# Kernel optimization log

Hardware: AMD Instinct MI355X
Metric: run time of the kernel (lower is better)

The kernel has to match this reference:

```python
import jax, jax.numpy as jnp
import numpy as np

B, T = 4, 15
NY = NX = 256
RES = 0.05
LAT0 = 32.0
G = 9.81
F0 = 1e-4
C0 = 2.7
DT = 21600.0
TINT = 86400.0
NSTEP = int(TINT // DT)  # 4 Euler sub-steps

# --- grid spacing: mean of dx, dy as in lonlat2dxdy (uniform lon/lat grid) ---
_lat = LAT0 + RES * np.arange(NX, dtype=np.float64)  # lat varies along axis 1
_dx_mean = RES * 111000.0
_dy_mean = RES * 111000.0 * np.mean(np.cos(np.deg2rad(_lat)))
DX = np.float32(0.5 * (_dx_mean + _dy_mean))

# --- Helmholtz operator in DST-I space, shape (NY-2, NX-2) (square grid) ---
_i = np.arange(1, NX - 1, dtype=np.float64)
_j = np.arange(1, NY - 1, dtype=np.float64)
_X, _Y = np.meshgrid(_i, _j, indexing='ij')
_lap = (2 * (np.cos(np.pi / (NX - 1) * _X) - 1) / DX**2
        + 2 * (np.cos(np.pi / (NY - 1) * _Y) - 1) / DX**2)
HELM = jnp.asarray((G / F0) * _lap - G * F0 / C0**2, dtype=jnp.float32)

# --- boundary masks (SSH=None -> no NaN land mask; ind0 is empty) ---
_m = np.full((NY, NX), 3, dtype=np.int32)
_m[0, :] = _m[:, 0] = _m[-1, :] = _m[:, -1] = 1
_m[1, 1:-1] = 2; _m[1:-1, 1] = 2
_m[-2, 1:-1] = 2; _m[-3, 1:-1] = 2
_m[1:-1, -2] = 2; _m[1:-1, -3] = 2
IND12 = jnp.asarray((_m == 1) | (_m == 2))


def dstI1D(x):
    """1D type-I discrete sine transform along last axis."""
    n = x.shape[-1]
    xp = jnp.pad(x, [(0, 0)] * (x.ndim - 1) + [(1, 1)])
    return jnp.fft.irfft(-1j * xp, norm='ortho')[..., 1:n + 1]


def dstI2D(x):
    return jnp.swapaxes(dstI1D(jnp.swapaxes(dstI1D(x), -1, -2)), -1, -2)


def h2uv(h):
    """SSH -> geostrophic (u, v). f is the constant F0."""
    u = jnp.zeros_like(h).at[..., 1:-1, 1:].set(
        -G / F0 * (h[..., 2:, :-1] + h[..., 2:, 1:] - h[..., :-2, 1:] - h[..., :-2, :-1]) / (4 * DX))
    v = jnp.zeros_like(h).at[..., 1:, 1:-1].set(
        G / F0 * (h[..., 1:, 2:] + h[..., :-1, 2:] - h[..., :-1, :-2] - h[..., 1:, :-2]) / (4 * DX))
    return u, v


def h2pv(h, hbc):
    """SSH -> potential vorticity with boundary values from hbc on ind1|ind2."""
    interior = (G / F0 * ((h[..., 2:, 1:-1] + h[..., :-2, 1:-1] - 2 * h[..., 1:-1, 1:-1]) / DX**2
                          + (h[..., 1:-1, 2:] + h[..., 1:-1, :-2] - 2 * h[..., 1:-1, 1:-1]) / DX**2)
                - G * F0 / C0**2 * h[..., 1:-1, 1:-1])
    q = jnp.zeros_like(h).at[..., 1:-1, 1:-1].set(interior)
    return jnp.where(IND12, -G * F0 / C0**2 * hbc, q)


def _adv(up, vp, um, vm, v0):
    """3rd-order upwind advection."""
    c = 1.0 / (6 * DX)
    inner = (
        -up[..., 1:-1, 1:-1] * c * (2 * v0[..., 2:-2, 3:-1] + 3 * v0[..., 2:-2, 2:-2] - 6 * v0[..., 2:-2, 1:-3] + v0[..., 2:-2, :-4])
        + um[..., 1:-1, 1:-1] * c * (v0[..., 2:-2, 4:] - 6 * v0[..., 2:-2, 3:-1] + 3 * v0[..., 2:-2, 2:-2] + 2 * v0[..., 2:-2, 1:-3])
        - vp[..., 1:-1, 1:-1] * c * (2 * v0[..., 3:-1, 2:-2] + 3 * v0[..., 2:-2, 2:-2] - 6 * v0[..., 1:-3, 2:-2] + v0[..., :-4, 2:-2])
        + vm[..., 1:-1, 1:-1] * c * (v0[..., 4:, 2:-2] - 6 * v0[..., 3:-1, 2:-2] + 3 * v0[..., 2:-2, 2:-2] + 2 * v0[..., 1:-3, 2:-2]))
    return jnp.zeros_like(v0).at[..., 2:-2, 2:-2].set(inner)


def rhs(u, v, q0, way=1.0):
    uT = way * 0.5 * (u[..., 1:-1, 1:-1] + u[..., 1:-1, 2:])
    vT = way * 0.5 * (v[..., 1:-1, 1:-1] + v[..., 2:, 1:-1])
    up = jnp.maximum(uT, 0.0); um = jnp.minimum(uT, 0.0)
    vp = jnp.maximum(vT, 0.0); vm = jnp.minimum(vT, 0.0)
    r = _adv(up, vp, um, vm, q0)
    # beta term is identically zero: f = F0 is spatially constant. Kdiffus=None.
    return jnp.where(IND12, 0.0, r)


def pv2h(q, hb, qb):
    """PV -> SSH via DST-based inverse Helmholtz solve."""
    qin = q[..., 1:-1, 1:-1] - qb[..., 1:-1, 1:-1]
    inv = dstI2D(dstI2D(qin) / HELM)
    return jnp.zeros_like(q).at[..., 1:-1, 1:-1].set(inv) + hb


def conv2d(x, w, b):
    y = jax.lax.conv_general_dilated(x, w, (1, 1), 'SAME',
                                     dimension_numbers=('NCHW', 'OIHW', 'NCHW'))
    return y + b[None, :, None, None]


def qg_forecast(x):
    """One-day QG forecast of each frame from the previous one (NSTEP Euler sub-steps)."""
    h0 = x[:, :-1]            # [B, T-1, NY, NX]
    hb = h0                    # background / boundary SSH
    qb = h2pv(hb, hb)

    def body(carry, _):
        h, q = carry
        u, v = h2uv(h)
        q1 = q + DT * rhs(u, v, q)
        h1 = pv2h(q1, hb, qb)
        return (h1, q1), None

    (hf, _), _ = jax.lax.scan(body, (h0, qb), None, length=NSTEP)
    return hf


def setup_inputs() -> dict:
    key = jax.random.key(0)
    ks = jax.random.split(key, 8)
    s = 0.05
    return {
        'x': jax.random.normal(ks[0], (B, T, NY, NX), jnp.float32),
        'w_in': s * jax.random.normal(ks[1], (64, T, 3, 3), jnp.float32),
        'b_in': jnp.zeros((64,), jnp.float32),
        'w_hid': s * jax.random.normal(ks[2], (64, 64, 3, 3), jnp.float32),
        'b_hid': jnp.zeros((64,), jnp.float32),
        'w_b1': s * jax.random.normal(ks[3], (64, 64, 3, 3), jnp.float32),
        'b_b1': jnp.zeros((64,), jnp.float32),
        'w_b21': s * jax.random.normal(ks[4], (64, 64, 3, 3), jnp.float32),
        'b_b21': jnp.zeros((64,), jnp.float32),
        'w_b22': s * jax.random.normal(ks[5], (64, 64, 3, 3), jnp.float32),
        'b_b22': jnp.zeros((64,), jnp.float32),
        'w_out': s * jax.random.normal(ks[6], (T, 128, 3, 3), jnp.float32),
        'b_out': jnp.zeros((T,), jnp.float32),
    }


def reference(x, w_in, b_in, w_hid, b_hid, w_b1, b_b1, w_b21, b_b21,
              w_b22, b_b22, w_out, b_out):
    # QG dynamical prior cost
    hf = qg_forecast(x)
    dyn_cost = jnp.mean((x[:, 1:] - hf) ** 2)
    # bilinear AE prior cost (bilin_quad=False -> product of two branches)
    z = conv2d(x, w_in, b_in)
    z = conv2d(jax.nn.relu(z), w_hid, b_hid)
    nonlin = conv2d(z, w_b21, b_b21) * conv2d(z, w_b22, b_b22)
    xa = conv2d(jnp.concatenate([conv2d(z, w_b1, b_b1), nonlin], axis=1), w_out, b_out)
    ae_cost = jnp.mean((x - xa) ** 2)
    return dyn_cost + ae_cost
```

## Files before the change

kernel.cpp:

```cpp
#include <hip/hip_runtime.h>
#include <math.h>

#define NS 56
#define NPIX 65536
#define NB_RED 1024

static constexpr double D_PI = 3.14159265358979323846;

typedef __attribute__((ext_vector_type(8))) short short8;
typedef __attribute__((ext_vector_type(4))) float f32x4;
typedef __attribute__((ext_vector_type(16))) float f32x16;

__device__ inline unsigned short f2bf(float f) {
  union { float f; unsigned int u; } v; v.f = f;
  unsigned int r = v.u + 0x7FFFu + ((v.u >> 16) & 1u);
  return (unsigned short)(r >> 16);
}
__device__ inline float bf2f(unsigned short b) {
  union { float f; unsigned int u; } v; v.u = ((unsigned int)b) << 16;
  return v.f;
}

#define OFF_PART 0
#define OFF_S    4096
#define OFF_HM   (OFF_S + 32768)
#define OFF_H    (OFF_HM + 65536)
#define SLC      (NS * NPIX)
#define OFF_Q0   (OFF_H + SLC)
#define OFF_Q1   (OFF_Q0 + SLC)
#define OFF_QB   (OFF_Q1 + SLC)
#define OFF_TA   (OFF_QB + SLC)
#define OFF_U    (OFF_TA + SLC / 2)
#define OFF_V    (OFF_U + SLC / 2)
#define OFF_XP   OFF_H
#define OFF_Z1   (OFF_XP + 2097152)
#define OFF_Z2   (OFF_Z1 + 8388608)
#define OFF_BC   (OFF_Z2 + 8388608)
#define OFF_XA   (OFF_BC + 8388608)
#define OFF_WT   (OFF_XA + 2097152)
#define W_IN    0
#define W_HID   10240
#define W_B1    47104
#define W_B21   83968
#define W_B22   120832
#define W_O1    157696
#define W_O2    166912

#define QCLAMP 1.0e12f
#define HCLAMP 1.0e15f

__global__ __launch_bounds__(256) void k_dst_init(unsigned short* __restrict__ S,
                                                  float* __restrict__ HM, float dx2f) {
  int idx = blockIdx.x * 256 + threadIdx.x;
  int i = idx >> 8, j = idx & 255;
  float sv = 0.f, hv = 1.f;
  if (i < 254 && j < 254) {
    double arg = D_PI * (double)((i + 1) * (j + 1)) / 255.0;
    sv = (float)((2.0 / sqrt(510.0)) * sin(arg));
    double la = 2.0 * (cos(D_PI * (double)(i + 1) / 255.0) - 1.0) / (double)dx2f
              + 2.0 * (cos(D_PI * (double)(j + 1) / 255.0) - 1.0) / (double)dx2f;
    hv = (float)((9.81 / 1e-4) * la - 9.81 * 1e-4 / (2.7 * 2.7));
  }
  S[idx] = f2bf(sv);
  HM[idx] = hv;
}

__global__ __launch_bounds__(256) void k_qg_init(const float* __restrict__ x,
                                                 float* __restrict__ h,
                                                 float* __restrict__ q,
                                                 float* __restrict__ qb,
                                                 float dx2, float gf, float gfc) {
  int idx = blockIdx.x * 256 + threadIdx.x;
  int s = idx >> 16, p = idx & 65535;
  int y = p >> 8, xx = p & 255;
  int b = s / 14, t = s - b * 14;
  const float* hb = x + (size_t)(b * 15 + t) * NPIX;
  float hc = hb[p];
  float qv;
  if (y >= 2 && y <= 252 && xx >= 2 && xx <= 252) {
    qv = gf * ((hb[p + 256] + hb[p - 256] - 2.f * hc) / dx2
             + (hb[p + 1] + hb[p - 1] - 2.f * hc) / dx2) - gfc * hc;
  } else {
    qv = -gfc * hc;
  }
  h[idx] = hc;
  q[idx] = qv;
  qb[idx] = qv;
}

__global__ __launch_bounds__(256) void k_qrhs(const float* __restrict__ h,
                                              const float* __restrict__ qc,
                                              const float* __restrict__ qb,
                                              float* __restrict__ qn,
                                              unsigned short* __restrict__ tA,
                                              float ngf, float pgf, float fdx,
                                              float cc, float dtf) {
  int idx = blockIdx.x * 256 + threadIdx.x;
  int s = idx >> 16, p = idx & 65535;
  int y = p >> 8, xx = p & 255;
  const float* H = h + (size_t)s * NPIX;
  const float* Q = qc + (size_t)s * NPIX;
  float qv = Q[p];
  float q1 = qv;
  if (y >= 2 && y <= 252 && xx >= 2 && xx <= 252) {
    float hSW = H[p + 255], hS = H[p + 256], hSE = H[p + 257];
    float hNW = H[p - 257], hN = H[p - 256], hNE = H[p - 255];
    float hW = H[p - 1], hE = H[p + 1];
    float uA = ngf * (hSW + hS - hN - hNW) / fdx;
    float uB = ngf * (hS + hSE - hNE - hN) / fdx;
    float vA = pgf * (hE + hNE - hNW - hW) / fdx;
    float vB = pgf * (hSE + hE - hW - hSW) / fdx;
    float uT = 0.5f * (uA + uB);
    float vT = 0.5f * (vA + vB);
    float up = fmaxf(uT, 0.f), um = fminf(uT, 0.f);
    float vp = fmaxf(vT, 0.f), vm = fminf(vT, 0.f);
    float Q0 = qv;
    float QE = Q[p + 1], QW = Q[p - 1], QEE = Q[p + 2], QWW = Q[p - 2];
    float QS = Q[p + 256], QN = Q[p - 256], QSS = Q[p + 512], QNN = Q[p - 512];
    float r = -up * cc * (2.f * QE + 3.f * Q0 - 6.f * QW + QWW)
            + um * cc * (QEE - 6.f * QE + 3.f * Q0 + 2.f * QW)
            - vp * cc * (2.f * QS + 3.f * Q0 - 6.f * QN + QNN)
            + vm * cc * (QSS - 6.f * QS + 3.f * Q0 + 2.f * QN);
    q1 = qv + dtf * r;
    q1 = fminf(fmaxf(q1, -QCLAMP), QCLAMP);
  }
  qn[idx] = q1;
  int wy = (y == 0) ? 254 : ((y == 255) ? 255 : y - 1);
  int wx = (xx == 0) ? 254 : ((xx == 255) ? 255 : xx - 1);
  float val = 0.f;
  if (y >= 1 && y <= 254 && xx >= 1 && xx <= 254) val = q1 - qb[idx];
  tA[(size_t)s * NPIX + wy * 256 + wx] = f2bf(val);
}

template <int EPI>
__global__ __launch_bounds__(512) void k_solve(const unsigned short* __restrict__ Sm,
                                               const unsigned short* __restrict__ Xb,
                                               unsigned short* __restrict__ Ob,
                                               const float* __restrict__ HM,
                                               const float* __restrict__ xin,
                                               float* __restrict__ hout) {
  __shared__ unsigned short Ul[32 * 256];
  const int s = blockIdx.x, q = blockIdx.y;
  const unsigned short* X = Xb + (size_t)s * NPIX;
  const int lane = threadIdx.x & 63, w = threadIdx.x >> 6;
  const int r31 = lane & 31, kh = lane >> 5;

  f32x16 acc;
#pragma unroll
  for (int i = 0; i < 16; ++i) acc[i] = 0.f;
  {
    const int ar = (32 * q + r31) * 256;
    const int br = (32 * w + r31) * 256;
#pragma unroll 4
    for (int kc = 0; kc < 256; kc += 16) {
      short8 a = *(const short8*)&Sm[ar + kc + kh * 8];
      short8 b = *(const short8*)&X[br + kc + kh * 8];
      acc = __builtin_amdgcn_mfma_f32_32x32x16_bf16(a, b, acc, 0, 0, 0);
    }
  }
  {
    const int col = 32 * w + r31;
    const int g = col >> 3, c7 = col & 7;
#pragma unroll
    for (int reg = 0; reg < 16; ++reg) {
      int i = (reg & 3) + 8 * (reg >> 2) + 4 * kh;
      Ul[i * 256 + (((g ^ (i & 7)) << 3) | c7)] = f2bf(acc[reg]);
    }
  }
  __syncthreads();

  f32x16 acc2;
#pragma unroll
  for (int i = 0; i < 16; ++i) acc2[i] = 0.f;
  {
    const int ar = (32 * w + r31) * 256;
    const int urow = r31 * 256;
    const int x7 = (r31 & 7);
#pragma unroll 4
    for (int kc = 0; kc < 256; kc += 16) {
      int g0 = (kc >> 3) + kh;
      short8 a = *(const short8*)&Sm[ar + kc + kh * 8];
      short8 b = *(const short8*)&Ul[urow + ((g0 ^ x7) << 3)];
      acc2 = __builtin_amdgcn_mfma_f32_32x32x16_bf16(a, b, acc2, 0, 0, 0);
    }
  }
  const int gn = 32 * q + r31;
  if (EPI == 0) {
    unsigned short* O = Ob + (size_t)s * NPIX;
#pragma unroll
    for (int reg = 0; reg < 16; ++reg) {
      int gm = 32 * w + (reg & 3) + 8 * (reg >> 2) + 4 * kh;
      O[(size_t)gm * 256 + gn] = f2bf(acc2[reg] / HM[(size_t)gm * 256 + gn]);
    }
  } else {
    int b = s / 14, t = s - b * 14;
    const float* hb = xin + (size_t)(b * 15 + t) * NPIX;
    float* H = hout + (size_t)s * NPIX;
    if (gn < 254) {
#pragma unroll
      for (int reg = 0; reg < 16; ++reg) {
        int gm = 32 * w + (reg & 3) + 8 * (reg >> 2) + 4 * kh;
        if (gm < 254) {
          size_t o = (size_t)(gm + 1) * 256 + (gn + 1);
          float hv = acc2[reg] + hb[o];
          H[o] = fminf(fmaxf(hv, -HCLAMP), HCLAMP);
        }
      }
    }
  }
}

__global__ __launch_bounds__(256) void k_pack_x(const float* __restrict__ x,
                                                unsigned short* __restrict__ xp) {
  int e = blockIdx.x * 256 + threadIdx.x;
  int b = e >> 16, p = e & 65535;
  const float* xb = x + (size_t)b * 15 * NPIX + p;
  union { unsigned short u16[16]; uint4 u4[2]; } vv;
#pragma unroll
  for (int c = 0; c < 15; ++c) vv.u16[c] = f2bf(xb[(size_t)c * NPIX]);
  vv.u16[15] = 0;
  uint4* dst = (uint4*)&xp[(size_t)e * 16];
  dst[0] = vv.u4[0];
  dst[1] = vv.u4[1];
}

__global__ __launch_bounds__(256) void k_wprep_all(const float* __restrict__ w_in,
                                                   const float* __restrict__ w_hid,
                                                   const float* __restrict__ w_b1,
                                                   const float* __restrict__ w_b21,
                                                   const float* __restrict__ w_b22,
                                                   const float* __restrict__ w_out,
                                                   unsigned short* __restrict__ wtb) {
  const int job = blockIdx.y;
  const float* src;
  int dstOff, chunks, icpShift, icw, ic0, icReal, ocw, ocReal;
  switch (job) {
    case 0: src = w_in;  dstOff = W_IN;  chunks = 5;  icpShift = 4; icw = 15;  ic0 = 0;  icReal = 15; ocw = 64; ocReal = 64; break;
    case 1: src = w_hid; dstOff = W_HID; chunks = 18; icpShift = 6; icw = 64;  ic0 = 0;  icReal = 64; ocw = 64; ocReal = 64; break;
    case 2: src = w_b1;  dstOff = W_B1;  chunks = 18; icpShift = 6; icw = 64;  ic0 = 0;  icReal = 64; ocw = 64; ocReal = 64; break;
    case 3: src = w_b21; dstOff = W_B21; chunks = 18; icpShift = 6; icw = 64;  ic0 = 0;  icReal = 64; ocw = 64; ocReal = 64; break;
    case 4: src = w_b22; dstOff = W_B22; chunks = 18; icpShift = 6; icw = 64;  ic0 = 0;  icReal = 64; ocw = 64; ocReal = 64; break;
    case 5: src = w_out; dstOff = W_O1;  chunks = 18; icpShift = 6; icw = 128; ic0 = 0;  icReal = 64; ocw = 16; ocReal = 15; break;
    default: src = w_out; dstOff = W_O2; chunks = 18; icpShift = 6; icw = 128; ic0 = 64; icReal = 64; ocw = 16; ocReal = 15; break;
  }
  int e = blockIdx.x * 256 + threadIdx.x;
  int total = chunks * 4 * ocw * 8;
  if (e >= total) return;
  int j = e & 7;
  int oc = (e >> 3) % ocw;
  int ckg = e / (8 * ocw);
  int kg = ckg & 3, c = ckg >> 2;
  int Kidx = c * 32 + kg * 8 + j;
  int tap = Kidx >> icpShift;
  int ic = Kidx & ((1 << icpShift) - 1);
  float v = 0.f;
  if (tap < 9 && ic < icReal && oc < ocReal)
    v = src[((size_t)oc * icw + ic0 + ic) * 9 + tap];
  wtb[dstOff + e] = f2bf(v);
}

template <int NSRC, int NOC, int OCF, bool RELU, int EMODE>
__global__ __launch_bounds__(256) void k_conv64(const unsigned short* __restrict__ in0,
                                                const unsigned short* __restrict__ in1,
                                                const unsigned short* __restrict__ wt,
                                                const float* __restrict__ bias, int ocReal,
                                                const unsigned short* __restrict__ other,
                                                unsigned short* __restrict__ out) {
  constexpr int OCW = NOC * 16;
  __shared__ unsigned short tile[324 * 64];

  const int tid = threadIdx.x;
  const int lane = tid & 63, wave = tid >> 6;
  const int cl = lane & 15, kg = lane >> 4;
  const int b = blockIdx.z;
  const int gx0 = blockIdx.x * 16, gy0 = blockIdx.y * 16;

  f32x4 acc[4][NOC];
#pragma unroll
  for (int j = 0; j < NOC; ++j) {
    int oc = j * 16 + cl;
    float bv = (bias != nullptr && oc < ocReal) ? bias[oc] : 0.f;
#pragma unroll
    for (int i = 0; i < 4; ++i) acc[i][j] = (f32x4){bv, bv, bv, bv};
  }

  for (int src = 0; src < NSRC; ++src) {
    const unsigned short* inb = (src ? in1 : in0) + (size_t)b * NPIX * 64;
    const unsigned short* wtp = wt + src * 36864;
    if (src) __syncthreads();
    for (int c = tid; c < 2592; c += 256) {
      int pp = c >> 3, g = c & 7;
      int ly = pp / 18, lx = pp - ly * 18;
      int iy = gy0 + ly - 1, ix = gx0 + lx - 1;
      uint4 v = make_uint4(0u, 0u, 0u, 0u);
      if (iy >= 0 && iy < 256 && ix >= 0 && ix < 256)
        v = *(const uint4*)&inb[((size_t)iy * 256 + ix) * 64 + g * 8];
      int sw = g ^ (pp & 7);
      *(uint4*)&tile[pp * 64 + sw * 8] = v;
    }
    __syncthreads();
#pragma unroll 3
    for (int cm = 0; cm < 18; ++cm) {
      const int tap = cm >> 1;
      const int g = (cm & 1) * 4 + kg;
      const int dy = tap / 3, dxx = tap - dy * 3;
      short8 bfr[NOC];
#pragma unroll
      for (int j = 0; j < NOC; ++j)
        bfr[j] = *(const short8*)&wtp[(((size_t)cm * 4 + kg) * OCW + j * 16 + cl) * 8];
      const int tc = cl + dxx;
#pragma unroll
      for (int i = 0; i < 4; ++i) {
        int pp = (wave * 4 + i + dy) * 18 + tc;
        int g2 = g ^ (pp & 7);
        short8 av = *(const short8*)&tile[pp * 64 + g2 * 8];
#pragma unroll
        for (int j = 0; j < NOC; ++j)
          acc[i][j] = __builtin_amdgcn_mfma_f32_16x16x32_bf16(av, bfr[j], acc[i][j], 0, 0, 0);
      }
    }
  }

  const size_t outBase = (size_t)b * NPIX * OCF;
#pragma unroll
  for (int i = 0; i < 4; ++i) {
    int y = gy0 + wave * 4 + i;
#pragma unroll
    for (int j = 0; j < NOC; ++j) {
      int oc = j * 16 + cl;
#pragma unroll
      for (int r = 0; r < 4; ++r) {
        int px = gx0 + kg * 4 + r;
        size_t oi = outBase + ((size_t)y * 256 + px) * OCF + oc;
        float v = acc[i][j][r];
        if (EMODE == 1) v *= bf2f(other[oi]);
        if (RELU) v = fmaxf(v, 0.f);
        out[oi] = f2bf(v);
      }
    }
  }
}

__global__ __launch_bounds__(256) void k_conv16(const unsigned short* __restrict__ in,
                                                const unsigned short* __restrict__ wt,
                                                const float* __restrict__ bias,
                                                unsigned short* __restrict__ out) {
  __shared__ unsigned short wlds[10240];
  __shared__ unsigned short tile[324 * 16];

  const int tid = threadIdx.x;
  const int lane = tid & 63, wave = tid >> 6;
  const int cl = lane & 15, kg = lane >> 4;
  const int b = blockIdx.z;
  const int gx0 = blockIdx.x * 16, gy0 = blockIdx.y * 16;

  {
    uint4* wl = (uint4*)wlds;
    const uint4* wg = (const uint4*)wt;
    for (int i = tid; i < 1280; i += 256) wl[i] = wg[i];
  }
  const unsigned short* inb = in + (size_t)b * NPIX * 16;
  for (int c = tid; c < 648; c += 256) {
    int pp = c >> 1, g = c & 1;
    int ly = pp / 18, lx = pp - ly * 18;
    int iy = gy0 + ly - 1, ix = gx0 + lx - 1;
    uint4 v = make_uint4(0u, 0u, 0u, 0u);
    if (iy >= 0 && iy < 256 && ix >= 0 && ix < 256)
      v = *(const uint4*)&inb[((size_t)iy * 256 + ix) * 16 + g * 8];
    int sw = g ^ (pp & 1);
    *(uint4*)&tile[pp * 16 + sw * 8] = v;
  }
  __syncthreads();

  f32x4 acc[4][4];
#pragma unroll
  for (int j = 0; j < 4; ++j) {
    float bv = bias[j * 16 + cl];
#pragma unroll
    for (int i = 0; i < 4; ++i) acc[i][j] = (f32x4){bv, bv, bv, bv};
  }

#pragma unroll
  for (int c = 0; c < 5; ++c) {
    int tap = 2 * c + (kg >> 1);
    int dy = tap / 3, dxx = tap - dy * 3;
    int gidx = kg & 1;
    short8 bfr[4];
#pragma unroll
    for (int j = 0; j < 4; ++j)
      bfr[j] = *(const short8*)&wlds[((c * 4 + kg) * 64 + j * 16 + cl) * 8];
    int tc = cl + dxx;
#pragma unroll
    for (int i = 0; i < 4; ++i) {
      int tr = wave * 4 + i + dy;
      if (tr > 17) tr = 17;
      int pp = tr * 18 + tc;
      int g2 = gidx ^ (pp & 1);
      short8 av = *(const short8*)&tile[pp * 16 + g2 * 8];
#pragma unroll
      for (int j = 0; j < 4; ++j)
        acc[i][j] = __builtin_amdgcn_mfma_f32_16x16x32_bf16(av, bfr[j], acc[i][j], 0, 0, 0);
    }
  }

  const size_t outBase = (size_t)b * NPIX * 64;
#pragma unroll
  for (int i = 0; i < 4; ++i) {
    int y = gy0 + wave * 4 + i;
#pragma unroll
    for (int j = 0; j < 4; ++j) {
      int oc = j * 16 + cl;
#pragma unroll
      for (int r = 0; r < 4; ++r) {
        int px = gx0 + kg * 4 + r;
        size_t oi = outBase + ((size_t)y * 256 + px) * 64 + oc;
        out[oi] = f2bf(fmaxf(acc[i][j][r], 0.f));
      }
    }
  }
}

__global__ __launch_bounds__(256) void k_red_dyn(const float* __restrict__ x,
                                                 const float* __restrict__ h,
                                                 double* __restrict__ part) {
  double sum = 0.0;
  for (int e = blockIdx.x * 256 + threadIdx.x; e < NS * NPIX; e += NB_RED * 256) {
    int s = e >> 16, p = e & 65535;
    int b = s / 14, t = s - b * 14;
    float d = x[(size_t)(b * 15 + t + 1) * NPIX + p] - h[e];
    sum += (double)d * (double)d;
  }
  for (int o = 32; o > 0; o >>= 1) sum += __shfl_down(sum, o);
  __shared__ double sw[4];
  int lane = threadIdx.x & 63, wid = threadIdx.x >> 6;
  if (lane == 0) sw[wid] = sum;
  __syncthreads();
  if (threadIdx.x == 0) part[blockIdx.x] = sw[0] + sw[1] + sw[2] + sw[3];
}

__global__ __launch_bounds__(256) void k_red_ae(const float* __restrict__ x,
                                                const unsigned short* __restrict__ xa,
                                                double* __restrict__ part) {
  double sum = 0.0;
  for (int e = blockIdx.x * 256 + threadIdx.x; e < 60 * NPIX; e += NB_RED * 256) {
    int b = e / (15 * NPIX);
    int r2 = e - b * 15 * NPIX;
    int c = r2 >> 16, p = r2 & 65535;
    float xav = bf2f(xa[((size_t)b * NPIX + p) * 16 + c]);
    float d = x[e] - xav;
    sum += (double)d * (double)d;
  }
  for (int o = 32; o > 0; o >>= 1) sum += __shfl_down(sum, o);
  __shared__ double sw[4];
  int lane = threadIdx.x & 63, wid = threadIdx.x >> 6;
  if (lane == 0) sw[wid] = sum;
  __syncthreads();
  if (threadIdx.x == 0) part[NB_RED + blockIdx.x] = sw[0] + sw[1] + sw[2] + sw[3];
}

__global__ __launch_bounds__(256) void k_final(const double* __restrict__ part,
                                               float* __restrict__ out) {
  double s1 = 0.0, s2 = 0.0;
  for (int i = threadIdx.x; i < NB_RED; i += 256) {
    s1 += part[i];
    s2 += part[NB_RED + i];
  }
  for (int o = 32; o > 0; o >>= 1) {
    s1 += __shfl_down(s1, o);
    s2 += __shfl_down(s2, o);
  }
  __shared__ double a1[4], a2[4];
  int lane = threadIdx.x & 63, wid = threadIdx.x >> 6;
  if (lane == 0) { a1[wid] = s1; a2[wid] = s2; }
  __syncthreads();
  if (threadIdx.x == 0) {
    double v = (a1[0] + a1[1] + a1[2] + a1[3]) / (double)(NS * NPIX)
             + (a2[0] + a2[1] + a2[2] + a2[3]) / (double)(60 * NPIX);
    if (!(v == v)) v = 0.0;
    if (v > 1.0e30) v = 1.0e30;
    if (v < -1.0e30) v = -1.0e30;
    out[0] = (float)v;
  }
}

extern "C" void kernel_launch(void* const* d_in, const int* in_sizes, int n_in,
                              void* d_out, int out_size, void* d_ws, size_t ws_size,
                              hipStream_t stream) {
  (void)in_sizes; (void)n_in; (void)out_size; (void)ws_size;
  const float* x     = (const float*)d_in[0];
  const float* w_in  = (const float*)d_in[1];
  const float* b_in  = (const float*)d_in[2];
  const float* w_hid = (const float*)d_in[3];
  const float* b_hid = (const float*)d_in[4];
  const float* w_b1  = (const float*)d_in[5];
  const float* b_b1  = (const float*)d_in[6];
  const float* w_b21 = (const float*)d_in[7];
  const float* b_b21 = (const float*)d_in[8];
  const float* w_b22 = (const float*)d_in[9];
  const float* b_b22 = (const float*)d_in[10];
  const float* w_out = (const float*)d_in[11];
  const float* b_out = (const float*)d_in[12];
  float* ws = (float*)d_ws;
  float* out = (float*)d_out;

  double mc = 0.0;
  for (int k = 0; k < 256; ++k) mc += cos((32.0 + 0.05 * k) * D_PI / 180.0);
  mc /= 256.0;
  float DXf = (float)(0.5 * (5550.0 + 5550.0 * mc));
  float dx2 = DXf * DXf;
  float gf  = (float)(9.81 / 1e-4);
  float ngf = (float)(-9.81 / 1e-4);
  float gfc = (float)(9.81 * 1e-4 / (2.7 * 2.7));
  float fdx = 4.0f * DXf;
  float cc  = 1.0f / (6.0f * DXf);
  float dtf = 21600.0f;

  double* part = (double*)d_ws;
  unsigned short* S  = (unsigned short*)(ws + OFF_S);
  float* HM = ws + OFF_HM;
  float* h  = ws + OFF_H;
  float* q0 = ws + OFF_Q0;
  float* q1 = ws + OFF_Q1;
  float* qb = ws + OFF_QB;
  unsigned short* tA = (unsigned short*)(ws + OFF_TA);
  unsigned short* A1 = (unsigned short*)(ws + OFF_U);
  unsigned short* wtb = (unsigned short*)(ws + OFF_WT);

  k_dst_init<<<dim3(256), dim3(256), 0, stream>>>(S, HM, dx2);
  k_wprep_all<<<dim3(144, 7), dim3(256), 0, stream>>>(w_in, w_hid, w_b1, w_b21, w_b22, w_out, wtb);
  k_qg_init<<<dim3(NS * NPIX / 256), dim3(256), 0, stream>>>(x, h, q0, qb, dx2, gf, gfc);

  float* qc = q0;
  float* qn = q1;
  dim3 sg(56, 8);
  for (int step = 0; step < 4; ++step) {
    k_qrhs<<<dim3(NS * NPIX / 256), dim3(256), 0, stream>>>(h, qc, qb, qn, tA,
                                                            ngf, gf, fdx, cc, dtf);
    k_solve<0><<<sg, dim3(512), 0, stream>>>(S, tA, A1, HM, nullptr, nullptr);
    k_solve<1><<<sg, dim3(512), 0, stream>>>(S, A1, nullptr, nullptr, x, h);
    float* tmp = qc; qc = qn; qn = tmp;
  }
  k_red_dyn<<<dim3(NB_RED), dim3(256), 0, stream>>>(x, h, part);

  unsigned short* xp = (unsigned short*)(ws + OFF_XP);
  unsigned short* z1 = (unsigned short*)(ws + OFF_Z1);
  unsigned short* z2 = (unsigned short*)(ws + OFF_Z2);
  unsigned short* bc = (unsigned short*)(ws + OFF_BC);
  unsigned short* xa = (unsigned short*)(ws + OFF_XA);

  k_pack_x<<<dim3(4 * NPIX / 256), dim3(256), 0, stream>>>(x, xp);

  dim3 cg4(16, 16, 4);
  k_conv16<<<cg4, dim3(256), 0, stream>>>(xp, wtb + W_IN, b_in, z1);
  k_conv64<1, 4, 64, false, 0><<<cg4, dim3(256), 0, stream>>>(
      z1, z1, wtb + W_HID, b_hid, 64, nullptr, z2);
  k_conv64<1, 4, 64, false, 0><<<cg4, dim3(256), 0, stream>>>(
      z2, z2, wtb + W_B1, b_b1, 64, nullptr, z1);
  k_conv64<1, 4, 64, false, 0><<<cg4, dim3(256), 0, stream>>>(
      z2, z2, wtb + W_B21, b_b21, 64, nullptr, bc);
  k_conv64<1, 4, 64, false, 1><<<cg4, dim3(256), 0, stream>>>(
      z2, z2, wtb + W_B22, b_b22, 64, bc, bc);
  k_conv64<2, 1, 16, false, 0><<<cg4, dim3(256), 0, stream>>>(
      z1, bc, wtb + W_O1, b_out, 15, nullptr, xa);

  k_red_ae<<<dim3(NB_RED), dim3(256), 0, stream>>>(x, xa, part);
  k_final<<<dim3(1), dim3(256), 0, stream>>>(part, out);
}
```

Baseline: 525.8 us.

## Fuse setup kernels, carry bf16 q-deltas, fuse bilinear convs and reductions

Merges the DST table init, weight prep, QG init and input packing into one preamble launch. The Euler loop no longer keeps full fp32 q arrays: it reconstructs q from the base PV plus the bf16 delta that the solve already consumes, which cuts memory traffic but stores the evolving q state at bf16 precision. The two bilinear-branch convolutions are fused into one kernel that shares the input tile and multiplies the results in registers, and the final reductions become a single kernel that finishes with a last-block atomic counter. The second-source weight stride of the output conv is also corrected from 36864 to 9216.

```diff
diff --git a/kernel.cpp b/kernel.cpp
--- a/kernel.cpp
+++ b/kernel.cpp
@@ -3,7 +3,6 @@
 
 #define NS 56
 #define NPIX 65536
-#define NB_RED 1024
 
 static constexpr double D_PI = 3.14159265358979323846;
 
@@ -21,18 +20,17 @@
   return v.f;
 }
 
+#define SLC      (NS * NPIX)
 #define OFF_PART 0
+#define OFF_CNT  3584
 #define OFF_S    4096
-#define OFF_HM   (OFF_S + 32768)
-#define OFF_H    (OFF_HM + 65536)
-#define SLC      (NS * NPIX)
-#define OFF_Q0   (OFF_H + SLC)
-#define OFF_Q1   (OFF_Q0 + SLC)
-#define OFF_QB   (OFF_Q1 + SLC)
-#define OFF_TA   (OFF_QB + SLC)
-#define OFF_U    (OFF_TA + SLC / 2)
-#define OFF_V    (OFF_U + SLC / 2)
-#define OFF_XP   OFF_H
+#define OFF_HM   36864
+#define OFF_H    102400
+#define OFF_QB   (OFF_H + SLC)
+#define OFF_DQ0  (OFF_QB + SLC)
+#define OFF_DQ1  (OFF_DQ0 + SLC / 2)
+#define OFF_A1   (OFF_DQ1 + SLC / 2)
+#define OFF_XP   (OFF_A1 + SLC / 2)
 #define OFF_Z1   (OFF_XP + 2097152)
 #define OFF_Z2   (OFF_Z1 + 8388608)
 #define OFF_BC   (OFF_Z2 + 8388608)
@@ -49,59 +47,115 @@
 #define QCLAMP 1.0e12f
 #define HCLAMP 1.0e15f
 
-__global__ __launch_bounds__(256) void k_dst_init(unsigned short* __restrict__ S,
-                                                  float* __restrict__ HM, float dx2f) {
-  int idx = blockIdx.x * 256 + threadIdx.x;
-  int i = idx >> 8, j = idx & 255;
-  float sv = 0.f, hv = 1.f;
-  if (i < 254 && j < 254) {
-    double arg = D_PI * (double)((i + 1) * (j + 1)) / 255.0;
-    sv = (float)((2.0 / sqrt(510.0)) * sin(arg));
-    double la = 2.0 * (cos(D_PI * (double)(i + 1) / 255.0) - 1.0) / (double)dx2f
-              + 2.0 * (cos(D_PI * (double)(j + 1) / 255.0) - 1.0) / (double)dx2f;
-    hv = (float)((9.81 / 1e-4) * la - 9.81 * 1e-4 / (2.7 * 2.7));
-  }
-  S[idx] = f2bf(sv);
-  HM[idx] = hv;
-}
-
-__global__ __launch_bounds__(256) void k_qg_init(const float* __restrict__ x,
-                                                 float* __restrict__ h,
-                                                 float* __restrict__ q,
-                                                 float* __restrict__ qb,
-                                                 float dx2, float gf, float gfc) {
-  int idx = blockIdx.x * 256 + threadIdx.x;
-  int s = idx >> 16, p = idx & 65535;
-  int y = p >> 8, xx = p & 255;
-  int b = s / 14, t = s - b * 14;
-  const float* hb = x + (size_t)(b * 15 + t) * NPIX;
-  float hc = hb[p];
-  float qv;
-  if (y >= 2 && y <= 252 && xx >= 2 && xx <= 252) {
-    qv = gf * ((hb[p + 256] + hb[p - 256] - 2.f * hc) / dx2
-             + (hb[p + 1] + hb[p - 1] - 2.f * hc) / dx2) - gfc * hc;
+__global__ __launch_bounds__(256) void k_preamble(const float* __restrict__ x,
+                                                  const float* __restrict__ w_in,
+                                                  const float* __restrict__ w_hid,
+                                                  const float* __restrict__ w_b1,
+                                                  const float* __restrict__ w_b21,
+                                                  const float* __restrict__ w_b22,
+                                                  const float* __restrict__ w_out,
+                                                  unsigned short* __restrict__ S,
+                                                  float* __restrict__ HM,
+                                                  unsigned short* __restrict__ wtb,
+                                                  float* __restrict__ h,
+                                                  float* __restrict__ qb,
+                                                  unsigned short* __restrict__ xp,
+                                                  unsigned int* __restrict__ cnt,
+                                                  float dx2, float gf, float gfc) {
+  const int blk = blockIdx.x;
+  const int tid = threadIdx.x;
+  if (blk < 256) {
+    int idx = blk * 256 + tid;
+    if (idx == 0) *cnt = 0u;
+    int i = idx >> 8, j = idx & 255;
+    float sv = 0.f, hv = 1.f;
+    if (i < 254 && j < 254) {
+      double arg = D_PI * (double)((i + 1) * (j + 1)) / 255.0;
+      sv = (float)((2.0 / sqrt(510.0)) * sin(arg));
+      double la = 2.0 * (cos(D_PI * (double)(i + 1) / 255.0) - 1.0) / (double)dx2
+                + 2.0 * (cos(D_PI * (double)(j + 1) / 255.0) - 1.0) / (double)dx2;
+      hv = (float)((9.81 / 1e-4) * la - 9.81 * 1e-4 / (2.7 * 2.7));
+    }
+    S[idx] = f2bf(sv);
+    HM[idx] = hv;
+  } else if (blk < 256 + 1008) {
+    int jb = blk - 256;
+    int job = jb / 144;
+    int e = (jb - job * 144) * 256 + tid;
+    const float* src;
+    int dstOff, chunks, icpShift, icw, ic0, icReal, ocw, ocReal;
+    switch (job) {
+      case 0: src = w_in;  dstOff = W_IN;  chunks = 5;  icpShift = 4; icw = 15;  ic0 = 0;  icReal = 15; ocw = 64; ocReal = 64; break;
+      case 1: src = w_hid; dstOff = W_HID; chunks = 18; icpShift = 6; icw = 64;  ic0 = 0;  icReal = 64; ocw = 64; ocReal = 64; break;
+      case 2: src = w_b1;  dstOff = W_B1;  chunks = 18; icpShift = 6; icw = 64;  ic0 = 0;  icReal = 64; ocw = 64; ocReal = 64; break;
+      case 3: src = w_b21; dstOff = W_B21; chunks = 18; icpShift = 6; icw = 64;  ic0 = 0;  icReal = 64; ocw = 64; ocReal = 64; break;
+      case 4: src = w_b22; dstOff = W_B22; chunks = 18; icpShift = 6; icw = 64;  ic0 = 0;  icReal = 64; ocw = 64; ocReal = 64; break;
+      case 5: src = w_out; dstOff = W_O1;  chunks = 18; icpShift = 6; icw = 128; ic0 = 0;  icReal = 64; ocw = 16; ocReal = 15; break;
+      default: src = w_out; dstOff = W_O2; chunks = 18; icpShift = 6; icw = 128; ic0 = 64; icReal = 64; ocw = 16; ocReal = 15; break;
+    }
+    int total = chunks * 4 * ocw * 8;
+    if (e < total) {
+      int j = e & 7;
+      int oc = (e >> 3) % ocw;
+      int ckg = e / (8 * ocw);
+      int kg = ckg & 3, c = ckg >> 2;
+      int Kidx = c * 32 + kg * 8 + j;
+      int tap = Kidx >> icpShift;
+      int ic = Kidx & ((1 << icpShift) - 1);
+      float v = 0.f;
+      if (tap < 9 && ic < icReal && oc < ocReal)
+        v = src[((size_t)oc * icw + ic0 + ic) * 9 + tap];
+      wtb[dstOff + e] = f2bf(v);
+    }
+  } else if (blk < 256 + 1008 + 14336) {
+    int idx = (blk - 1264) * 256 + tid;
+    int s = idx >> 16, p = idx & 65535;
+    int y = p >> 8, xx = p & 255;
+    int b = s / 14, t = s - b * 14;
+    const float* hb = x + (size_t)(b * 15 + t) * NPIX;
+    float hc = hb[p];
+    float qv;
+    if (y >= 2 && y <= 252 && xx >= 2 && xx <= 252) {
+      qv = gf * ((hb[p + 256] + hb[p - 256] - 2.f * hc) / dx2
+               + (hb[p + 1] + hb[p - 1] - 2.f * hc) / dx2) - gfc * hc;
+    } else {
+      qv = -gfc * hc;
+    }
+    h[idx] = hc;
+    qb[idx] = qv;
   } else {
-    qv = -gfc * hc;
-  }
-  h[idx] = hc;
-  q[idx] = qv;
-  qb[idx] = qv;
-}
-
-__global__ __launch_bounds__(256) void k_qrhs(const float* __restrict__ h,
-                                              const float* __restrict__ qc,
-                                              const float* __restrict__ qb,
-                                              float* __restrict__ qn,
-                                              unsigned short* __restrict__ tA,
-                                              float ngf, float pgf, float fdx,
-                                              float cc, float dtf) {
+    int e = (blk - 15600) * 256 + tid;
+    int b = e >> 16, p = e & 65535;
+    const float* xb = x + (size_t)b * 15 * NPIX + p;
+    union { unsigned short u16[16]; uint4 u4[2]; } vv;
+#pragma unroll
+    for (int c = 0; c < 15; ++c) vv.u16[c] = f2bf(xb[(size_t)c * NPIX]);
+    vv.u16[15] = 0;
+    uint4* dst = (uint4*)&xp[(size_t)e * 16];
+    dst[0] = vv.u4[0];
+    dst[1] = vv.u4[1];
+  }
+}
+
+template <bool FIRST>
+__global__ __launch_bounds__(256) void k_qrhs_dq(const float* __restrict__ h,
+                                                 const float* __restrict__ qbb,
+                                                 const unsigned short* __restrict__ dqin,
+                                                 unsigned short* __restrict__ dqout,
+                                                 float ngf, float pgf, float fdx,
+                                                 float cc, float dtf) {
   int idx = blockIdx.x * 256 + threadIdx.x;
   int s = idx >> 16, p = idx & 65535;
   int y = p >> 8, xx = p & 255;
   const float* H = h + (size_t)s * NPIX;
-  const float* Q = qc + (size_t)s * NPIX;
-  float qv = Q[p];
-  float q1 = qv;
+  const float* QB = qbb + (size_t)s * NPIX;
+  const unsigned short* DQ = FIRST ? nullptr : dqin + (size_t)s * NPIX;
+  auto dq = [&](int yy, int xc) -> float {
+    if (FIRST) return 0.f;
+    if (yy < 1 || yy > 254 || xc < 1 || xc > 254) return 0.f;
+    return bf2f(DQ[(yy - 1) * 256 + (xc - 1)]);
+  };
+  float q1mqb = 0.f;
   if (y >= 2 && y <= 252 && xx >= 2 && xx <= 252) {
     float hSW = H[p + 255], hS = H[p + 256], hSE = H[p + 257];
     float hNW = H[p - 257], hN = H[p - 256], hNE = H[p - 255];
@@ -114,22 +168,23 @@
     float vT = 0.5f * (vA + vB);
     float up = fmaxf(uT, 0.f), um = fminf(uT, 0.f);
     float vp = fmaxf(vT, 0.f), vm = fminf(vT, 0.f);
-    float Q0 = qv;
-    float QE = Q[p + 1], QW = Q[p - 1], QEE = Q[p + 2], QWW = Q[p - 2];
-    float QS = Q[p + 256], QN = Q[p - 256], QSS = Q[p + 512], QNN = Q[p - 512];
+    float qbc = QB[p];
+    float Q0 = qbc + dq(y, xx);
+    float QE = QB[p + 1] + dq(y, xx + 1), QW = QB[p - 1] + dq(y, xx - 1);
+    float QEE = QB[p + 2] + dq(y, xx + 2), QWW = QB[p - 2] + dq(y, xx - 2);
+    float QS = QB[p + 256] + dq(y + 1, xx), QN = QB[p - 256] + dq(y - 1, xx);
+    float QSS = QB[p + 512] + dq(y + 2, xx), QNN = QB[p - 512] + dq(y - 2, xx);
     float r = -up * cc * (2.f * QE + 3.f * Q0 - 6.f * QW + QWW)
             + um * cc * (QEE - 6.f * QE + 3.f * Q0 + 2.f * QW)
             - vp * cc * (2.f * QS + 3.f * Q0 - 6.f * QN + QNN)
             + vm * cc * (QSS - 6.f * QS + 3.f * Q0 + 2.f * QN);
-    q1 = qv + dtf * r;
+    float q1 = Q0 + dtf * r;
     q1 = fminf(fmaxf(q1, -QCLAMP), QCLAMP);
-  }
-  qn[idx] = q1;
+    q1mqb = q1 - qbc;
+  }
   int wy = (y == 0) ? 254 : ((y == 255) ? 255 : y - 1);
   int wx = (xx == 0) ? 254 : ((xx == 255) ? 255 : xx - 1);
-  float val = 0.f;
-  if (y >= 1 && y <= 254 && xx >= 1 && xx <= 254) val = q1 - qb[idx];
-  tA[(size_t)s * NPIX + wy * 256 + wx] = f2bf(val);
+  dqout[(size_t)s * NPIX + wy * 256 + wx] = f2bf(q1mqb);
 }
 
 template <int EPI>
@@ -210,56 +265,7 @@
   }
 }
 
-__global__ __launch_bounds__(256) void k_pack_x(const float* __restrict__ x,
-                                                unsigned short* __restrict__ xp) {
-  int e = blockIdx.x * 256 + threadIdx.x;
-  int b = e >> 16, p = e & 65535;
-  const float* xb = x + (size_t)b * 15 * NPIX + p;
-  union { unsigned short u16[16]; uint4 u4[2]; } vv;
-#pragma unroll
-  for (int c = 0; c < 15; ++c) vv.u16[c] = f2bf(xb[(size_t)c * NPIX]);
-  vv.u16[15] = 0;
-  uint4* dst = (uint4*)&xp[(size_t)e * 16];
-  dst[0] = vv.u4[0];
-  dst[1] = vv.u4[1];
-}
-
-__global__ __launch_bounds__(256) void k_wprep_all(const float* __restrict__ w_in,
-                                                   const float* __restrict__ w_hid,
-                                                   const float* __restrict__ w_b1,
-                                                   const float* __restrict__ w_b21,
-                                                   const float* __restrict__ w_b22,
-                                                   const float* __restrict__ w_out,
-                                                   unsigned short* __restrict__ wtb) {
-  const int job = blockIdx.y;
-  const float* src;
-  int dstOff, chunks, icpShift, icw, ic0, icReal, ocw, ocReal;
-  switch (job) {
-    case 0: src = w_in;  dstOff = W_IN;  chunks = 5;  icpShift = 4; icw = 15;  ic0 = 0;  icReal = 15; ocw = 64; ocReal = 64; break;
-    case 1: src = w_hid; dstOff = W_HID; chunks = 18; icpShift = 6; icw = 64;  ic0 = 0;  icReal = 64; ocw = 64; ocReal = 64; break;
-    case 2: src = w_b1;  dstOff = W_B1;  chunks = 18; icpShift = 6; icw = 64;  ic0 = 0;  icReal = 64; ocw = 64; ocReal = 64; break;
-    case 3: src = w_b21; dstOff = W_B21; chunks = 18; icpShift = 6; icw = 64;  ic0 = 0;  icReal = 64; ocw = 64; ocReal = 64; break;
-    case 4: src = w_b22; dstOff = W_B22; chunks = 18; icpShift = 6; icw = 64;  ic0 = 0;  icReal = 64; ocw = 64; ocReal = 64; break;
-    case 5: src = w_out; dstOff = W_O1;  chunks = 18; icpShift = 6; icw = 128; ic0 = 0;  icReal = 64; ocw = 16; ocReal = 15; break;
-    default: src = w_out; dstOff = W_O2; chunks = 18; icpShift = 6; icw = 128; ic0 = 64; icReal = 64; ocw = 16; ocReal = 15; break;
-  }
-  int e = blockIdx.x * 256 + threadIdx.x;
-  int total = chunks * 4 * ocw * 8;
-  if (e >= total) return;
-  int j = e & 7;
-  int oc = (e >> 3) % ocw;
-  int ckg = e / (8 * ocw);
-  int kg = ckg & 3, c = ckg >> 2;
-  int Kidx = c * 32 + kg * 8 + j;
-  int tap = Kidx >> icpShift;
-  int ic = Kidx & ((1 << icpShift) - 1);
-  float v = 0.f;
-  if (tap < 9 && ic < icReal && oc < ocReal)
-    v = src[((size_t)oc * icw + ic0 + ic) * 9 + tap];
-  wtb[dstOff + e] = f2bf(v);
-}
-
-template <int NSRC, int NOC, int OCF, bool RELU, int EMODE>
+template <int NSRC, int NOC, int OCF, bool RELU, int EMODE, int WSTRIDE>
 __global__ __launch_bounds__(256) void k_conv64(const unsigned short* __restrict__ in0,
                                                 const unsigned short* __restrict__ in1,
                                                 const unsigned short* __restrict__ wt,
@@ -286,7 +292,7 @@
 
   for (int src = 0; src < NSRC; ++src) {
     const unsigned short* inb = (src ? in1 : in0) + (size_t)b * NPIX * 64;
-    const unsigned short* wtp = wt + src * 36864;
+    const unsigned short* wtp = wt + src * WSTRIDE;
     if (src) __syncthreads();
     for (int c = tid; c < 2592; c += 256) {
       int pp = c >> 3, g = c & 7;
@@ -341,6 +347,89 @@
   }
 }
 
+__global__ __launch_bounds__(256) void k_convmul(const unsigned short* __restrict__ in,
+                                                 const unsigned short* __restrict__ wtA,
+                                                 const unsigned short* __restrict__ wtB,
+                                                 const float* __restrict__ biasA,
+                                                 const float* __restrict__ biasB,
+                                                 unsigned short* __restrict__ out) {
+  __shared__ unsigned short tile[324 * 64];
+  const int tid = threadIdx.x;
+  const int lane = tid & 63, wave = tid >> 6;
+  const int cl = lane & 15, kg = lane >> 4;
+  const int b = blockIdx.z;
+  const int gx0 = blockIdx.x * 16, gy0 = blockIdx.y * 16;
+
+  f32x4 accA[4][4], accB[4][4];
+#pragma unroll
+  for (int j = 0; j < 4; ++j) {
+    float ba = biasA[j * 16 + cl], bb = biasB[j * 16 + cl];
+#pragma unroll
+    for (int i = 0; i < 4; ++i) {
+      accA[i][j] = (f32x4){ba, ba, ba, ba};
+      accB[i][j] = (f32x4){bb, bb, bb, bb};
+    }
+  }
+
+  const unsigned short* inb = in + (size_t)b * NPIX * 64;
+  for (int c = tid; c < 2592; c += 256) {
+    int pp = c >> 3, g = c & 7;
+    int ly = pp / 18, lx = pp - ly * 18;
+    int iy = gy0 + ly - 1, ix = gx0 + lx - 1;
+    uint4 v = make_uint4(0u, 0u, 0u, 0u);
+    if (iy >= 0 && iy < 256 && ix >= 0 && ix < 256)
+      v = *(const uint4*)&inb[((size_t)iy * 256 + ix) * 64 + g * 8];
+    int sw = g ^ (pp & 7);
+    *(uint4*)&tile[pp * 64 + sw * 8] = v;
+  }
+  __syncthreads();
+
+#pragma unroll 2
+  for (int cm = 0; cm < 18; ++cm) {
+    const int tap = cm >> 1;
+    const int g = (cm & 1) * 4 + kg;
+    const int dy = tap / 3, dxx = tap - dy * 3;
+    const int tc = cl + dxx;
+    short8 av[4];
+#pragma unroll
+    for (int i = 0; i < 4; ++i) {
+      int pp = (wave * 4 + i + dy) * 18 + tc;
+      int g2 = g ^ (pp & 7);
+      av[i] = *(const short8*)&tile[pp * 64 + g2 * 8];
+    }
+#pragma unroll
+    for (int j = 0; j < 4; ++j) {
+      short8 wa = *(const short8*)&wtA[(((size_t)cm * 4 + kg) * 64 + j * 16 + cl) * 8];
+#pragma unroll
+      for (int i = 0; i < 4; ++i)
+        accA[i][j] = __builtin_amdgcn_mfma_f32_16x16x32_bf16(av[i], wa, accA[i][j], 0, 0, 0);
+    }
+#pragma unroll
+    for (int j = 0; j < 4; ++j) {
+      short8 wb = *(const short8*)&wtB[(((size_t)cm * 4 + kg) * 64 + j * 16 + cl) * 8];
+#pragma unroll
+      for (int i = 0; i < 4; ++i)
+        accB[i][j] = __builtin_amdgcn_mfma_f32_16x16x32_bf16(av[i], wb, accB[i][j], 0, 0, 0);
+    }
+  }
+
+  const size_t outBase = (size_t)b * NPIX * 64;
+#pragma unroll
+  for (int i = 0; i < 4; ++i) {
+    int y = gy0 + wave * 4 + i;
+#pragma unroll
+    for (int j = 0; j < 4; ++j) {
+      int oc = j * 16 + cl;
+#pragma unroll
+      for (int r = 0; r < 4; ++r) {
+        int px = gx0 + kg * 4 + r;
+        size_t oi = outBase + ((size_t)y * 256 + px) * 64 + oc;
+        out[oi] = f2bf(accA[i][j][r] * accB[i][j][r]);
+      }
+    }
+  }
+}
+
 __global__ __launch_bounds__(256) void k_conv16(const unsigned short* __restrict__ in,
                                                 const unsigned short* __restrict__ wt,
                                                 const float* __restrict__ bias,
@@ -420,66 +509,67 @@
   }
 }
 
-__global__ __launch_bounds__(256) void k_red_dyn(const float* __restrict__ x,
+__global__ __launch_bounds__(256) void k_red_all(const float* __restrict__ x,
                                                  const float* __restrict__ h,
-                                                 double* __restrict__ part) {
+                                                 const unsigned short* __restrict__ xa,
+                                                 double* __restrict__ part,
+                                                 unsigned int* __restrict__ cnt,
+                                                 float* __restrict__ out) {
+  const int NB1 = 1024, NBT = 1536;
+  const int bid = blockIdx.x;
+  const int tid = threadIdx.x;
   double sum = 0.0;
-  for (int e = blockIdx.x * 256 + threadIdx.x; e < NS * NPIX; e += NB_RED * 256) {
-    int s = e >> 16, p = e & 65535;
-    int b = s / 14, t = s - b * 14;
-    float d = x[(size_t)(b * 15 + t + 1) * NPIX + p] - h[e];
-    sum += (double)d * (double)d;
+  if (bid < NB1) {
+    for (int e = bid * 256 + tid; e < NS * NPIX; e += NB1 * 256) {
+      int s = e >> 16, p = e & 65535;
+      int b = s / 14, t = s - b * 14;
+      float d = x[(size_t)(b * 15 + t + 1) * NPIX + p] - h[e];
+      sum += (double)d * (double)d;
+    }
+  } else {
+    for (int e = (bid - NB1) * 256 + tid; e < 60 * NPIX; e += (NBT - NB1) * 256) {
+      int b = e / (15 * NPIX);
+      int r2 = e - b * 15 * NPIX;
+      int c = r2 >> 16, p = r2 & 65535;
+      float xav = bf2f(xa[((size_t)b * NPIX + p) * 16 + c]);
+      float d = x[e] - xav;
+      sum += (double)d * (double)d;
+    }
   }
   for (int o = 32; o > 0; o >>= 1) sum += __shfl_down(sum, o);
   __shared__ double sw[4];
-  int lane = threadIdx.x & 63, wid = threadIdx.x >> 6;
+  __shared__ bool last;
+  int lane = tid & 63, wid = tid >> 6;
   if (lane == 0) sw[wid] = sum;
   __syncthreads();
-  if (threadIdx.x == 0) part[blockIdx.x] = sw[0] + sw[1] + sw[2] + sw[3];
-}
-
-__global__ __launch_bounds__(256) void k_red_ae(const float* __restrict__ x,
-                                                const unsigned short* __restrict__ xa,
-                                                double* __restrict__ part) {
-  double sum = 0.0;
-  for (int e = blockIdx.x * 256 + threadIdx.x; e < 60 * NPIX; e += NB_RED * 256) {
-    int b = e / (15 * NPIX);
-    int r2 = e - b * 15 * NPIX;
-    int c = r2 >> 16, p = r2 & 65535;
-    float xav = bf2f(xa[((size_t)b * NPIX + p) * 16 + c]);
-    float d = x[e] - xav;
-    sum += (double)d * (double)d;
-  }
-  for (int o = 32; o > 0; o >>= 1) sum += __shfl_down(sum, o);
-  __shared__ double sw[4];
-  int lane = threadIdx.x & 63, wid = threadIdx.x >> 6;
-  if (lane == 0) sw[wid] = sum;
+  if (tid == 0) {
+    part[bid] = sw[0] + sw[1] + sw[2] + sw[3];
+    __threadfence();
+    unsigned int t = atomicAdd(cnt, 1u);
+    last = (t == (unsigned)(NBT - 1));
+  }
   __syncthreads();
-  if (threadIdx.x == 0) part[NB_RED + blockIdx.x] = sw[0] + sw[1] + sw[2] + sw[3];
-}
-
-__global__ __launch_bounds__(256) void k_final(const double* __restrict__ part,
-                                               float* __restrict__ out) {
-  double s1 = 0.0, s2 = 0.0;
-  for (int i = threadIdx.x; i < NB_RED; i += 256) {
-    s1 += part[i];
-    s2 += part[NB_RED + i];
-  }
-  for (int o = 32; o > 0; o >>= 1) {
-    s1 += __shfl_down(s1, o);
-    s2 += __shfl_down(s2, o);
-  }
-  __shared__ double a1[4], a2[4];
-  int lane = threadIdx.x & 63, wid = threadIdx.x >> 6;
-  if (lane == 0) { a1[wid] = s1; a2[wid] = s2; }
-  __syncthreads();
-  if (threadIdx.x == 0) {
-    double v = (a1[0] + a1[1] + a1[2] + a1[3]) / (double)(NS * NPIX)
-             + (a2[0] + a2[1] + a2[2] + a2[3]) / (double)(60 * NPIX);
-    if (!(v == v)) v = 0.0;
-    if (v > 1.0e30) v = 1.0e30;
-    if (v < -1.0e30) v = -1.0e30;
-    out[0] = (float)v;
+  if (last) {
+    __threadfence();
+    double s1 = 0.0, s2 = 0.0;
+    for (int i = tid; i < NBT; i += 256) {
+      if (i < NB1) s1 += part[i]; else s2 += part[i];
+    }
+    for (int o = 32; o > 0; o >>= 1) {
+      s1 += __shfl_down(s1, o);
+      s2 += __shfl_down(s2, o);
+    }
+    __shared__ double a1[4], a2[4];
+    if (lane == 0) { a1[wid] = s1; a2[wid] = s2; }
+    __syncthreads();
+    if (tid == 0) {
+      double v = (a1[0] + a1[1] + a1[2] + a1[3]) / (double)(NS * NPIX)
+               + (a2[0] + a2[1] + a2[2] + a2[3]) / (double)(60 * NPIX);
+      if (!(v == v)) v = 0.0;
+      if (v > 1.0e30) v = 1.0e30;
+      if (v < -1.0e30) v = -1.0e30;
+      out[0] = (float)v;
+    }
   }
 }
 
@@ -516,53 +606,49 @@
   float dtf = 21600.0f;
 
   double* part = (double*)d_ws;
+  unsigned int* cnt = (unsigned int*)(ws + OFF_CNT);
   unsigned short* S  = (unsigned short*)(ws + OFF_S);
   float* HM = ws + OFF_HM;
   float* h  = ws + OFF_H;
-  float* q0 = ws + OFF_Q0;
-  float* q1 = ws + OFF_Q1;
   float* qb = ws + OFF_QB;
-  unsigned short* tA = (unsigned short*)(ws + OFF_TA);
-  unsigned short* A1 = (unsigned short*)(ws + OFF_U);
-  unsigned short* wtb = (unsigned short*)(ws + OFF_WT);
-
-  k_dst_init<<<dim3(256), dim3(256), 0, stream>>>(S, HM, dx2);
-  k_wprep_all<<<dim3(144, 7), dim3(256), 0, stream>>>(w_in, w_hid, w_b1, w_b21, w_b22, w_out, wtb);
-  k_qg_init<<<dim3(NS * NPIX / 256), dim3(256), 0, stream>>>(x, h, q0, qb, dx2, gf, gfc);
-
-  float* qc = q0;
-  float* qn = q1;
-  dim3 sg(56, 8);
-  for (int step = 0; step < 4; ++step) {
-    k_qrhs<<<dim3(NS * NPIX / 256), dim3(256), 0, stream>>>(h, qc, qb, qn, tA,
-                                                            ngf, gf, fdx, cc, dtf);
-    k_solve<0><<<sg, dim3(512), 0, stream>>>(S, tA, A1, HM, nullptr, nullptr);
-    k_solve<1><<<sg, dim3(512), 0, stream>>>(S, A1, nullptr, nullptr, x, h);
-    float* tmp = qc; qc = qn; qn = tmp;
-  }
-  k_red_dyn<<<dim3(NB_RED), dim3(256), 0, stream>>>(x, h, part);
-
+  unsigned short* dq0 = (unsigned short*)(ws + OFF_DQ0);
+  unsigned short* dq1 = (unsigned short*)(ws + OFF_DQ1);
+  unsigned short* A1 = (unsigned short*)(ws + OFF_A1);
   unsigned short* xp = (unsigned short*)(ws + OFF_XP);
   unsigned short* z1 = (unsigned short*)(ws + OFF_Z1);
   unsigned short* z2 = (unsigned short*)(ws + OFF_Z2);
   unsigned short* bc = (unsigned short*)(ws + OFF_BC);
   unsigned short* xa = (unsigned short*)(ws + OFF_XA);
-
-  k_pack_x<<<dim3(4 * NPIX / 256), dim3(256), 0, stream>>>(x, xp);
+  unsigned short* wtb = (unsigned short*)(ws + OFF_WT);
+
+  k_preamble<<<dim3(16624), dim3(256), 0, stream>>>(x, w_in, w_hid, w_b1, w_b21, w_b22,
+                                                    w_out, S, HM, wtb, h, qb, xp, cnt,
+                                                    dx2, gf, gfc);
+
+  dim3 sg(56, 8);
+  dim3 qg(NS * NPIX / 256);
+  unsigned short* dqc = dq0;
+  unsigned short* dqn = dq1;
+  for (int step = 0; step < 4; ++step) {
+    if (step == 0)
+      k_qrhs_dq<true><<<qg, dim3(256), 0, stream>>>(h, qb, nullptr, dqc, ngf, gf, fdx, cc, dtf);
+    else {
+      k_qrhs_dq<false><<<qg, dim3(256), 0, stream>>>(h, qb, dqc, dqn, ngf, gf, fdx, cc, dtf);
+      unsigned short* tmp = dqc; dqc = dqn; dqn = tmp;
+    }
+    k_solve<0><<<sg, dim3(512), 0, stream>>>(S, dqc, A1, HM, nullptr, nullptr);
+    k_solve<1><<<sg, dim3(512), 0, stream>>>(S, A1, nullptr, nullptr, x, h);
+  }
 
   dim3 cg4(16, 16, 4);
   k_conv16<<<cg4, dim3(256), 0, stream>>>(xp, wtb + W_IN, b_in, z1);
-  k_conv64<1, 4, 64, false, 0><<<cg4, dim3(256), 0, stream>>>(
+  k_conv64<1, 4, 64, false, 0, 0><<<cg4, dim3(256), 0, stream>>>(
       z1, z1, wtb + W_HID, b_hid, 64, nullptr, z2);
-  k_conv64<1, 4, 64, false, 0><<<cg4, dim3(256), 0, stream>>>(
+  k_conv64<1, 4, 64, false, 0, 0><<<cg4, dim3(256), 0, stream>>>(
       z2, z2, wtb + W_B1, b_b1, 64, nullptr, z1);
-  k_conv64<1, 4, 64, false, 0><<<cg4, dim3(256), 0, stream>>>(
-      z2, z2, wtb + W_B21, b_b21, 64, nullptr, bc);
-  k_conv64<1, 4, 64, false, 1><<<cg4, dim3(256), 0, stream>>>(
-      z2, z2, wtb + W_B22, b_b22, 64, bc, bc);
-  k_conv64<2, 1, 16, false, 0><<<cg4, dim3(256), 0, stream>>>(
+  k_convmul<<<cg4, dim3(256), 0, stream>>>(z2, wtb + W_B21, wtb + W_B22, b_b21, b_b22, bc);
+  k_conv64<2, 1, 16, false, 0, 9216><<<cg4, dim3(256), 0, stream>>>(
       z1, bc, wtb + W_O1, b_out, 15, nullptr, xa);
 
-  k_red_ae<<<dim3(NB_RED), dim3(256), 0, stream>>>(x, xa, part);
-  k_final<<<dim3(1), dim3(256), 0, stream>>>(part, out);
-}
+  k_red_all<<<dim3(1536), dim3(256), 0, stream>>>(x, h, xa, part, cnt, out);
+}
```

Result: slower. 555.5 us (+5.6%).
